# Kernel optimization log

Hardware: AMD Instinct MI355X
Metric: run time of the kernel (lower is better)

The kernel has to match this reference:

```python
import jax, jax.numpy as jnp
import numpy as np

B, H, W, C = 8, 28, 28, 1024
NH = 16
HD = C // NH
HID = 4 * C
BC = C // 2
SCALE = HD ** -0.5
EPS_LN = 1e-5   # nn.LayerNorm default
EPS_CLN = 1e-6  # detectron2 LayerNorm default


def layer_norm(x, w, b, eps=EPS_LN):
    m = jnp.mean(x, -1, keepdims=True)
    v = jnp.mean((x - m) ** 2, -1, keepdims=True)
    return (x - m) * jax.lax.rsqrt(v + eps) * w + b


def conv2d(x, w, padding):
    return jax.lax.conv_general_dilated(x, w, (1, 1), padding,
                                        dimension_numbers=("NHWC", "HWIO", "NHWC"))


def rel_table(rel_pos, size):
    # q_size == k_size, so relative index is simply (i - j) + (size - 1)
    idx = jnp.arange(size)[:, None] - jnp.arange(size)[None, :] + (size - 1)
    return rel_pos[idx]  # (size, size, HD)


def setup_inputs() -> dict:
    key = jax.random.key(0)
    ks = jax.random.split(key, 12)
    rn = lambda k, shape, s=0.02: jax.random.normal(k, shape, jnp.float32) * s
    return {
        "x": jax.random.normal(ks[0], (B, H, W, C), jnp.float32),
        "ln1_w": jnp.ones((C,), jnp.float32), "ln1_b": jnp.zeros((C,), jnp.float32),
        "qkv_w": rn(ks[1], (C, 3 * C)), "qkv_b": jnp.zeros((3 * C,), jnp.float32),
        "proj_w": rn(ks[2], (C, C)), "proj_b": jnp.zeros((C,), jnp.float32),
        "rel_pos_h": rn(ks[3], (2 * H - 1, HD)),
        "rel_pos_w": rn(ks[4], (2 * W - 1, HD)),
        "ln2_w": jnp.ones((C,), jnp.float32), "ln2_b": jnp.zeros((C,), jnp.float32),
        "mlp_w1": rn(ks[5], (C, HID)), "mlp_b1": jnp.zeros((HID,), jnp.float32),
        "mlp_w2": rn(ks[6], (HID, C)), "mlp_b2": jnp.zeros((C,), jnp.float32),
        "conv1_w": rn(ks[7], (1, 1, C, BC)),
        "cln1_w": jnp.ones((BC,), jnp.float32), "cln1_b": jnp.zeros((BC,), jnp.float32),
        "conv2_w": rn(ks[8], (3, 3, BC, BC)),
        "cln2_w": jnp.ones((BC,), jnp.float32), "cln2_b": jnp.zeros((BC,), jnp.float32),
        "conv3_w": rn(ks[9], (1, 1, BC, C)),
        "cln3_w": jnp.ones((C,), jnp.float32), "cln3_b": jnp.zeros((C,), jnp.float32),
    }


def _attention(h, qkv_w, qkv_b, proj_w, proj_b, rel_pos_h, rel_pos_w):
    # h: (B, N, C) with N = H*W
    Bq, N, _ = h.shape
    qkv = (h @ qkv_w + qkv_b).reshape(Bq, N, 3, NH, HD)
    q, k, v = jnp.moveaxis(qkv, 2, 0)          # each (B, N, NH, HD)
    q = jnp.swapaxes(q, 1, 2)                  # (B, NH, N, HD)
    k = jnp.swapaxes(k, 1, 2)
    v = jnp.swapaxes(v, 1, 2)
    attn = jnp.einsum("bhqd,bhkd->bhqk", q * SCALE, k)  # (B, NH, N, N)
    # decomposed relative position bias (uses UNscaled q, as in torch source)
    Rh = rel_table(rel_pos_h, H)               # (H, H, HD)
    Rw = rel_table(rel_pos_w, W)               # (W, W, HD)
    rq = q.reshape(Bq, NH, H, W, HD)
    rel_h = jnp.einsum("bnhwd,hkd->bnhwk", rq, Rh)  # (B, NH, H, W, H)
    rel_w = jnp.einsum("bnhwd,wkd->bnhwk", rq, Rw)  # (B, NH, H, W, W)
    attn = (attn.reshape(Bq, NH, H, W, H, W)
            + rel_h[..., :, None] + rel_w[..., None, :]).reshape(Bq, NH, N, N)
    attn = jax.nn.softmax(attn, axis=-1)
    out = jnp.einsum("bhqk,bhkd->bhqd", attn, v)     # (B, NH, N, HD)
    out = jnp.swapaxes(out, 1, 2).reshape(Bq, N, C)
    return out @ proj_w + proj_b


def reference(x, ln1_w, ln1_b, qkv_w, qkv_b, proj_w, proj_b, rel_pos_h, rel_pos_w,
              ln2_w, ln2_b, mlp_w1, mlp_b1, mlp_w2, mlp_b2,
              conv1_w, cln1_w, cln1_b, conv2_w, cln2_w, cln2_b,
              conv3_w, cln3_w, cln3_b):
    Bq = x.shape[0]
    N = H * W
    xt = x.reshape(Bq, N, C)
    shortcut = xt
    h = layer_norm(xt, ln1_w, ln1_b)
    a = _attention(h, qkv_w, qkv_b, proj_w, proj_b, rel_pos_h, rel_pos_w)
    xt = shortcut + a
    h2 = layer_norm(xt, ln2_w, ln2_b)
    mlp = jax.nn.gelu(h2 @ mlp_w1 + mlp_b1, approximate=False) @ mlp_w2 + mlp_b2
    xt = xt + mlp
    y = xt.reshape(Bq, H, W, C)
    # residual bottleneck conv block (NHWC; detectron2 LN == per-pixel channel LN)
    o = conv2d(y, conv1_w, "VALID")
    o = jax.nn.gelu(layer_norm(o, cln1_w, cln1_b, EPS_CLN), approximate=False)
    o = conv2d(o, conv2_w, "SAME")
    o = jax.nn.gelu(layer_norm(o, cln2_w, cln2_b, EPS_CLN), approximate=False)
    o = conv2d(o, conv3_w, "VALID")
    o = layer_norm(o, cln3_w, cln3_b, EPS_CLN)
    return y + o
```

## Files before the change

kernel.cpp:

```cpp
#include <hip/hip_runtime.h>
#include <hip/hip_bf16.h>

#define DI __device__ __forceinline__

typedef short bf16x8 __attribute__((ext_vector_type(8)));
typedef float f32x4 __attribute__((ext_vector_type(4)));

constexpr int BB = 8, CC = 1024, NHEAD = 16, HD = 64, HIDC = 4096, BCC = 512;
constexpr int NT = 784;
constexpr int MROWS = BB * NT;
constexpr float ATT_SCALE = 0.125f;

DI short f2bf(float f) {
    unsigned u = __builtin_bit_cast(unsigned, f);
    u = u + 0x7FFFu + ((u >> 16) & 1u);
    return (short)(u >> 16);
}
DI float bf2f(short h) {
    unsigned u = ((unsigned)(unsigned short)h) << 16;
    return __builtin_bit_cast(float, u);
}
DI float gelu_f(float x) { return 0.5f * x * (1.0f + erff(x * 0.70710678118654752f)); }

DI void gload16(const void* g, void* l) {
    __builtin_amdgcn_global_load_lds(
        (const __attribute__((address_space(1))) void*)g,
        (__attribute__((address_space(3))) void*)l, 16, 0, 0);
}

__global__ __launch_bounds__(256)
void cvt_t_kernel(const float* __restrict__ in, short* __restrict__ out, int K, int N) {
    __shared__ short t[64][68];
    const int k0 = blockIdx.y * 64, n0 = blockIdx.x * 64;
    const int tid = threadIdx.x;
    const int r = tid >> 4, c4 = (tid & 15) << 2;
    #pragma unroll
    for (int rr = 0; rr < 64; rr += 16) {
        float4 v = *(const float4*)(in + (size_t)(k0 + r + rr) * N + n0 + c4);
        t[r + rr][c4 + 0] = f2bf(v.x); t[r + rr][c4 + 1] = f2bf(v.y);
        t[r + rr][c4 + 2] = f2bf(v.z); t[r + rr][c4 + 3] = f2bf(v.w);
    }
    __syncthreads();
    #pragma unroll
    for (int rr = 0; rr < 64; rr += 16) {
        int nrow = r + rr;
        short4 o;
        o.x = t[c4 + 0][nrow]; o.y = t[c4 + 1][nrow];
        o.z = t[c4 + 2][nrow]; o.w = t[c4 + 3][nrow];
        *(short4*)(out + (size_t)(n0 + nrow) * K + k0 + c4) = o;
    }
}

__global__ void cvt_tables_kernel(const float* __restrict__ rph, const float* __restrict__ rpw,
                                  short* __restrict__ rhb, short* __restrict__ rwb) {
    int i = blockIdx.x * 256 + threadIdx.x;
    if (i < 3520) rhb[i] = f2bf(rph[i]);
    else if (i < 7040) rwb[i - 3520] = f2bf(rpw[i - 3520]);
}

template<bool GELU_, bool RESID, bool OUTBF>
__global__ void ln_kernel(const float* __restrict__ in, const float* __restrict__ gw,
                          const float* __restrict__ gb, const float* __restrict__ resid,
                          void* __restrict__ outv, int C, float eps) {
    const int row = blockIdx.x;
    const int tid = threadIdx.x;
    const float* x = in + (size_t)row * C;
    const int c4 = C >> 2;
    float s = 0.f, s2 = 0.f;
    for (int i = tid; i < c4; i += 256) {
        float4 v = ((const float4*)x)[i];
        s += v.x + v.y + v.z + v.w;
        s2 += v.x * v.x + v.y * v.y + v.z * v.z + v.w * v.w;
    }
    for (int off = 32; off; off >>= 1) { s += __shfl_xor(s, off); s2 += __shfl_xor(s2, off); }
    __shared__ float sa[4], sb[4], stats[2];
    int wid = tid >> 6;
    if ((tid & 63) == 0) { sa[wid] = s; sb[wid] = s2; }
    __syncthreads();
    if (tid == 0) {
        float S = sa[0] + sa[1] + sa[2] + sa[3];
        float S2 = sb[0] + sb[1] + sb[2] + sb[3];
        float mean = S / C;
        float var = S2 / C - mean * mean;
        stats[0] = mean; stats[1] = rsqrtf(var + eps);
    }
    __syncthreads();
    const float mean = stats[0], rstd = stats[1];
    for (int i = tid; i < c4; i += 256) {
        float4 v = ((const float4*)x)[i];
        float4 w4 = ((const float4*)gw)[i];
        float4 b4 = ((const float4*)gb)[i];
        float o[4] = { (v.x - mean) * rstd * w4.x + b4.x,
                       (v.y - mean) * rstd * w4.y + b4.y,
                       (v.z - mean) * rstd * w4.z + b4.z,
                       (v.w - mean) * rstd * w4.w + b4.w };
        if (GELU_) {
            #pragma unroll
            for (int j = 0; j < 4; j++) o[j] = gelu_f(o[j]);
        }
        if (RESID) {
            float4 r4 = ((const float4*)(resid + (size_t)row * C))[i];
            o[0] += r4.x; o[1] += r4.y; o[2] += r4.z; o[3] += r4.w;
        }
        if (OUTBF) {
            short4 ov; ov.x = f2bf(o[0]); ov.y = f2bf(o[1]); ov.z = f2bf(o[2]); ov.w = f2bf(o[3]);
            ((short4*)((short*)outv + (size_t)row * C))[i] = ov;
        } else {
            float4 ov; ov.x = o[0]; ov.y = o[1]; ov.z = o[2]; ov.w = o[3];
            ((float4*)((float*)outv + (size_t)row * C))[i] = ov;
        }
    }
}

template<bool OUTBF, bool HASB, bool ACTG, bool HASR, bool IMC, bool DUAL>
__global__ __launch_bounds__(256)
void gemm_kernel(const short* __restrict__ A, const short* __restrict__ Bt,
                 const float* __restrict__ bias, const float* __restrict__ resid,
                 void* __restrict__ outv, short* __restrict__ out2,
                 int M, int N, int K, const short* __restrict__ zg) {
    __shared__ __align__(16) short As[128 * 32];
    __shared__ __align__(16) short Bs[128 * 32];
    const int tid = threadIdx.x;
    const int nwg = gridDim.x * gridDim.y;
    const int orig = blockIdx.y * gridDim.x + blockIdx.x;
    const int qq = nwg >> 3, rr8 = nwg & 7;
    const int xcd = orig & 7, loc = orig >> 3;
    const int wg = (xcd < rr8 ? xcd * (qq + 1) : rr8 * (qq + 1) + (xcd - rr8) * qq) + loc;
    const int m0 = (wg / gridDim.x) * 128, n0 = (wg % gridDim.x) * 128;
    const int lane = tid & 63, wid = tid >> 6;
    const int wr = (wid >> 1) * 64, wc = (wid & 1) * 64;
    const int lr = lane & 15, lkb = lane >> 4;

    const int srow = lane >> 2;
    const int schunk = lane & 3;

    const short* aptr[2];
    const short* bptr[2];
    short* adst[2]; short* bdst[2];
    int ihh[2], iww[2], ioff[2];
    const short* ibase[2];

    #pragma unroll
    for (int i = 0; i < 2; i++) {
        int seg = wid * 2 + i;
        int row = seg * 16 + srow;
        int c = schunk ^ (row & 3);
        adst[i] = As + seg * 512;
        bdst[i] = Bs + seg * 512;
        bptr[i] = Bt + (size_t)(n0 + row) * K + c * 8;
        if (!IMC) {
            aptr[i] = A + (size_t)(m0 + row) * K + c * 8;
        } else {
            int m = m0 + row;
            int bimg = m / 784, rem = m - bimg * 784;
            ihh[i] = rem / 28; iww[i] = rem - (rem / 28) * 28;
            ibase[i] = A + (size_t)bimg * 784 * 512;
            ioff[i] = c * 8;
        }
    }

    f32x4 acc[4][4];
    #pragma unroll
    for (int i = 0; i < 4; i++)
        #pragma unroll
        for (int j = 0; j < 4; j++) acc[i][j] = f32x4{0.f, 0.f, 0.f, 0.f};

    const int pc = (lkb ^ (lr & 3)) << 3;
    const int nkt = K >> 5;
    for (int kt = 0; kt < nkt; ++kt) {
        if (!IMC) {
            #pragma unroll
            for (int i = 0; i < 2; i++) {
                gload16(aptr[i] + kt * 32, adst[i]);
                gload16(bptr[i] + kt * 32, bdst[i]);
            }
        } else {
            int segk = kt >> 4;
            int ky = segk / 3, kx = segk - ky * 3;
            int ccb = (kt & 15) << 5;
            #pragma unroll
            for (int i = 0; i < 2; i++) {
                int ih = ihh[i] + ky - 1, iw = iww[i] + kx - 1;
                bool ok = (ih >= 0) & (ih < 28) & (iw >= 0) & (iw < 28);
                const short* s = ok ? ibase[i] + ((size_t)(ih * 28 + iw) * 512 + ccb + ioff[i]) : zg;
                gload16(s, adst[i]);
                gload16(bptr[i] + kt * 32, bdst[i]);
            }
        }
        __syncthreads();
        bf16x8 af[4], bfv[4];
        #pragma unroll
        for (int mt = 0; mt < 4; mt++) af[mt] = *(const bf16x8*)&As[(wr + mt * 16 + lr) * 32 + pc];
        #pragma unroll
        for (int nt = 0; nt < 4; nt++) bfv[nt] = *(const bf16x8*)&Bs[(wc + nt * 16 + lr) * 32 + pc];
        #pragma unroll
        for (int mt = 0; mt < 4; mt++)
            #pragma unroll
            for (int nt = 0; nt < 4; nt++)
                acc[mt][nt] = __builtin_amdgcn_mfma_f32_16x16x32_bf16(af[mt], bfv[nt], acc[mt][nt], 0, 0, 0);
        __syncthreads();
    }
    const int ro = (lane >> 4) << 2;
    #pragma unroll
    for (int mt = 0; mt < 4; mt++) {
        #pragma unroll
        for (int nt = 0; nt < 4; nt++) {
            int col = n0 + wc + nt * 16 + lr;
            float bv = HASB ? bias[col] : 0.0f;
            #pragma unroll
            for (int j = 0; j < 4; j++) {
                int row = m0 + wr + mt * 16 + ro + j;
                float v = acc[mt][nt][j] + bv;
                if (ACTG) v = gelu_f(v);
                size_t oi = (size_t)row * N + col;
                if (HASR) v += resid[oi];
                if (OUTBF) ((short*)outv)[oi] = f2bf(v);
                else       ((float*)outv)[oi] = v;
                if (DUAL)  out2[oi] = f2bf(v);
            }
        }
    }
}

__global__ __launch_bounds__(64)
void relpos_mfma_kernel(const short* __restrict__ qkv, const short* __restrict__ rhb,
                        const short* __restrict__ rwb, float* __restrict__ relh,
                        float* __restrict__ relw) {
    const int p = blockIdx.x;
    const int bh = blockIdx.y;
    const int mode = blockIdx.z;
    const int bimg = bh >> 4, nh = bh & 15;
    const int lane = threadIdx.x;
    const int lr = lane & 15, lkb = lane >> 4;
    const short* rb = mode ? rwb : rhb;
    float* outp = mode ? relw : relh;

    bf16x8 afr[2][2];
    #pragma unroll
    for (int mt = 0; mt < 2; mt++) {
        int kh = mt * 16 + lr;
        int sr = p - kh + 27;
        sr = sr < 0 ? 0 : (sr > 54 ? 54 : sr);
        #pragma unroll
        for (int ks = 0; ks < 2; ks++)
            afr[mt][ks] = *(const bf16x8*)(rb + sr * 64 + ks * 32 + lkb * 8);
    }
    bf16x8 bfq[2][2];
    #pragma unroll
    for (int nt = 0; nt < 2; nt++) {
        int cc = nt * 16 + lr;
        int nlin = mode ? (cc * 28 + p) : (p * 28 + cc);
        if (nlin > 783) nlin = 783;
        const short* qp = qkv + (size_t)(bimg * 784 + nlin) * 3072 + nh * 64;
        #pragma unroll
        for (int ks = 0; ks < 2; ks++)
            bfq[nt][ks] = *(const bf16x8*)(qp + ks * 32 + lkb * 8);
    }
    f32x4 acc[2][2];
    #pragma unroll
    for (int i = 0; i < 2; i++)
        #pragma unroll
        for (int j = 0; j < 2; j++) acc[i][j] = f32x4{0.f, 0.f, 0.f, 0.f};
    #pragma unroll
    for (int ks = 0; ks < 2; ks++)
        #pragma unroll
        for (int mt = 0; mt < 2; mt++)
            #pragma unroll
            for (int nt = 0; nt < 2; nt++)
                acc[mt][nt] = __builtin_amdgcn_mfma_f32_16x16x32_bf16(afr[mt][ks], bfq[nt][ks], acc[mt][nt], 0, 0, 0);
    const int ro = lkb << 2;
    #pragma unroll
    for (int nt = 0; nt < 2; nt++) {
        int cc = nt * 16 + lr;
        if (cc < 28) {
            int nlin = mode ? (cc * 28 + p) : (p * 28 + cc);
            float* o = outp + ((size_t)bh * 784 + nlin) * 28;
            *(f32x4*)(o + ro) = acc[0][nt];
            if (ro < 12) *(f32x4*)(o + 16 + ro) = acc[1][nt];
        }
    }
}

__global__ __launch_bounds__(256)
void attn_kernel(const short* __restrict__ qkv, const float* __restrict__ relh,
                 const float* __restrict__ relw, short* __restrict__ outp) {
    constexpr int VSTR = 34;
    __shared__ __align__(16) short Ks[32 * 64];
    __shared__ __align__(16) short Vt[64 * VSTR];
    __shared__ __align__(16) short Pl[4][16 * 40];
    __shared__ float relS[4][16 * 57];
    const int qb = blockIdx.x;
    const int bh = blockIdx.y;
    const int bimg = bh >> 4, nh = bh & 15;
    const int tid = threadIdx.x;
    const int lane = tid & 63, wid = tid >> 6;
    const int lr = lane & 15, lkb = lane >> 4;
    const int lk = lkb * 8;
    const int qw0 = qb * 64 + wid * 16;

    for (int idx = lane; idx < 16 * 56; idx += 64) {
        int qq = idx / 56, j = idx - qq * 56;
        int n = qw0 + qq; if (n > 783) n = 783;
        relS[wid][qq * 57 + j] = (j < 28) ? relh[((size_t)bh * 784 + n) * 28 + j]
                                          : relw[((size_t)bh * 784 + n) * 28 + (j - 28)];
    }
    bf16x8 bq0, bq1;
    {
        int tok = qw0 + lr; if (tok > 783) tok = 783;
        const short* qp = qkv + (size_t)(bimg * 784 + tok) * 3072 + nh * 64;
        bq0 = *(const bf16x8*)(qp + lk);
        bq1 = *(const bf16x8*)(qp + 32 + lk);
    }
    f32x4 oacc[4];
    #pragma unroll
    for (int i = 0; i < 4; i++) oacc[i] = f32x4{0.f, 0.f, 0.f, 0.f};
    float m_run = -1e30f, l_run = 0.0f;

    const int krow = tid >> 3, kcp = tid & 7;
    const int kclog = kcp ^ (krow & 7);
    short* kdst = Ks + wid * 512;
    const int vkey = tid & 31, vdb = tid >> 5;
    const int kq4 = lkb << 2;

    for (int kt = 0; kt < 25; ++kt) {
        const int k0 = kt * 32;
        {
            int key = k0 + krow; if (key > 783) key = 783;
            gload16(qkv + (size_t)(bimg * 784 + key) * 3072 + 1024 + nh * 64 + kclog * 8, kdst);
        }
        {
            int key = k0 + vkey; if (key > 783) key = 783;
            bf16x8 vv = *(const bf16x8*)(qkv + (size_t)(bimg * 784 + key) * 3072 + 2048 + nh * 64 + vdb * 8);
            #pragma unroll
            for (int j = 0; j < 8; j++) Vt[(vdb * 8 + j) * VSTR + vkey] = vv[j];
        }
        __syncthreads();
        f32x4 sacc[2];
        sacc[0] = f32x4{0.f, 0.f, 0.f, 0.f}; sacc[1] = f32x4{0.f, 0.f, 0.f, 0.f};
        #pragma unroll
        for (int mb = 0; mb < 2; mb++) {
            int row = mb * 16 + lr;
            bf16x8 ak0 = *(const bf16x8*)&Ks[row * 64 + ((lkb ^ (row & 7)) << 3)];
            bf16x8 ak1 = *(const bf16x8*)&Ks[row * 64 + (((4 + lkb) ^ (row & 7)) << 3)];
            sacc[mb] = __builtin_amdgcn_mfma_f32_16x16x32_bf16(ak0, bq0, sacc[mb], 0, 0, 0);
            sacc[mb] = __builtin_amdgcn_mfma_f32_16x16x32_bf16(ak1, bq1, sacc[mb], 0, 0, 0);
        }
        float sv[8];
        #pragma unroll
        for (int mb = 0; mb < 2; mb++)
            #pragma unroll
            for (int j = 0; j < 4; j++) {
                int key = k0 + mb * 16 + kq4 + j;
                float v;
                if (key < 784) {
                    int h2 = key / 28, w2 = key - (key / 28) * 28;
                    v = sacc[mb][j] * ATT_SCALE + relS[wid][lr * 57 + h2] + relS[wid][lr * 57 + 28 + w2];
                } else v = -1e30f;
                sv[mb * 4 + j] = v;
            }
        float mt_ = sv[0];
        #pragma unroll
        for (int i = 1; i < 8; i++) mt_ = fmaxf(mt_, sv[i]);
        mt_ = fmaxf(mt_, __shfl_xor(mt_, 16));
        mt_ = fmaxf(mt_, __shfl_xor(mt_, 32));
        if (__all(mt_ - m_run <= 8.0f)) {
            float psum = 0.f;
            #pragma unroll
            for (int i = 0; i < 8; i++) {
                float pz = __expf(sv[i] - m_run);
                psum += pz;
                Pl[wid][lr * 40 + ((i >> 2) * 16 + kq4 + (i & 3))] = f2bf(pz);
            }
            psum += __shfl_xor(psum, 16);
            psum += __shfl_xor(psum, 32);
            l_run += psum;
        } else {
            float mnew = fmaxf(m_run, mt_);
            float corr = __expf(m_run - mnew);
            float psum = 0.f;
            #pragma unroll
            for (int i = 0; i < 8; i++) {
                float pz = __expf(sv[i] - mnew);
                psum += pz;
                Pl[wid][lr * 40 + ((i >> 2) * 16 + kq4 + (i & 3))] = f2bf(pz);
            }
            psum += __shfl_xor(psum, 16);
            psum += __shfl_xor(psum, 32);
            l_run = l_run * corr + psum;
            m_run = mnew;
            #pragma unroll
            for (int db = 0; db < 4; db++) {
                f32x4 t = oacc[db];
                t[0] *= corr; t[1] *= corr; t[2] *= corr; t[3] *= corr;
                oacc[db] = t;
            }
        }
        bf16x8 pb = *(const bf16x8*)&Pl[wid][lr * 40 + lk];
        #pragma unroll
        for (int db = 0; db < 4; db++) {
            bf16x8 av = *(const bf16x8*)&Vt[(db * 16 + lr) * VSTR + lk];
            oacc[db] = __builtin_amdgcn_mfma_f32_16x16x32_bf16(av, pb, oacc[db], 0, 0, 0);
        }
        __syncthreads();
    }
    const float inv = 1.0f / l_run;
    const int tok = qw0 + lr;
    if (tok < 784) {
        short* op = outp + (size_t)(bimg * 784 + tok) * 1024 + nh * 64;
        #pragma unroll
        for (int db = 0; db < 4; db++)
            #pragma unroll
            for (int j = 0; j < 4; j++) {
                int d = db * 16 + kq4 + j;
                op[d] = f2bf(oacc[db][j] * inv);
            }
    }
}

extern "C" void kernel_launch(void* const* d_in, const int* in_sizes, int n_in,
                              void* d_out, int out_size, void* d_ws, size_t ws_size,
                              hipStream_t stream) {
    const float* x      = (const float*)d_in[0];
    const float* ln1w   = (const float*)d_in[1];
    const float* ln1b   = (const float*)d_in[2];
    const float* qkvw   = (const float*)d_in[3];
    const float* qkvbia = (const float*)d_in[4];
    const float* projw  = (const float*)d_in[5];
    const float* projb  = (const float*)d_in[6];
    const float* rph    = (const float*)d_in[7];
    const float* rpw    = (const float*)d_in[8];
    const float* ln2w   = (const float*)d_in[9];
    const float* ln2b   = (const float*)d_in[10];
    const float* m1w    = (const float*)d_in[11];
    const float* m1b    = (const float*)d_in[12];
    const float* m2w    = (const float*)d_in[13];
    const float* m2b    = (const float*)d_in[14];
    const float* c1w    = (const float*)d_in[15];
    const float* cl1w   = (const float*)d_in[16];
    const float* cl1b   = (const float*)d_in[17];
    const float* c2w    = (const float*)d_in[18];
    const float* cl2w   = (const float*)d_in[19];
    const float* cl2b   = (const float*)d_in[20];
    const float* c3w    = (const float*)d_in[21];
    const float* cl3w   = (const float*)d_in[22];
    const float* cl3b   = (const float*)d_in[23];
    float* out = (float*)d_out;

    char* base = (char*)d_ws;
    size_t off = 0;
    auto alloc = [&](size_t bytes) -> char* {
        char* p = base + off;
        off = (off + bytes + 255) & ~(size_t)255;
        return p;
    };
    short* wq  = (short*)alloc((size_t)3072 * 1024 * 2);
    short* wp  = (short*)alloc((size_t)1024 * 1024 * 2);
    short* w1  = (short*)alloc((size_t)4096 * 1024 * 2);
    short* w2  = (short*)alloc((size_t)1024 * 4096 * 2);
    short* wc1 = (short*)alloc((size_t)512 * 1024 * 2);
    short* wc2 = (short*)alloc((size_t)512 * 4608 * 2);
    short* wc3 = (short*)alloc((size_t)1024 * 512 * 2);
    short* hbuf = (short*)alloc((size_t)MROWS * 1024 * 2);
    short* qkvb = (short*)alloc((size_t)MROWS * 3072 * 2);
    float* relh = (float*)alloc((size_t)128 * 784 * 28 * 4);
    float* relw = (float*)alloc((size_t)128 * 784 * 28 * 4);
    float* xt   = (float*)alloc((size_t)MROWS * 1024 * 4);
    short* hid  = (short*)alloc((size_t)MROWS * 4096 * 2);
    float* yf   = (float*)alloc((size_t)MROWS * 1024 * 4);
    short* zg   = (short*)alloc(256);
    short* rhb  = (short*)alloc(3520 * 2);
    short* rwb  = (short*)alloc(3520 * 2);
    (void)relw; (void)ws_size; (void)in_sizes; (void)n_in; (void)out_size;

    float* o1f  = (float*)hid;
    short* o1g  = (short*)((char*)hid + (size_t)MROWS * 512 * 4);
    float* o2f  = (float*)((char*)o1g + (size_t)MROWS * 512 * 2);
    short* o2g  = (short*)((char*)o2f + (size_t)MROWS * 512 * 4);
    float* o3f  = (float*)qkvb;
    short* ybf  = (short*)relh;

    hipMemsetAsync(zg, 0, 256, stream);

    auto cvtT = [&](const float* src, short* dst, int K, int N) {
        cvt_t_kernel<<<dim3(N / 64, K / 64), 256, 0, stream>>>(src, dst, K, N);
    };
    cvtT(qkvw, wq, 1024, 3072);
    cvtT(projw, wp, 1024, 1024);
    cvtT(m1w, w1, 1024, 4096);
    cvtT(m2w, w2, 4096, 1024);
    cvtT(c1w, wc1, 1024, 512);
    cvtT(c2w, wc2, 4608, 512);
    cvtT(c3w, wc3, 512, 1024);
    cvt_tables_kernel<<<28, 256, 0, stream>>>(rph, rpw, rhb, rwb);

    ln_kernel<false, false, true><<<MROWS, 256, 0, stream>>>(x, ln1w, ln1b, nullptr, hbuf, 1024, 1e-5f);
    gemm_kernel<true, true, false, false, false, false><<<dim3(24, 49), 256, 0, stream>>>(
        hbuf, wq, qkvbia, nullptr, qkvb, nullptr, MROWS, 3072, 1024, zg);
    relpos_mfma_kernel<<<dim3(28, 128, 2), 64, 0, stream>>>(qkvb, rhb, rwb, relh, relw);
    attn_kernel<<<dim3(13, 128), 256, 0, stream>>>(qkvb, relh, relw, hbuf);
    gemm_kernel<false, true, false, true, false, false><<<dim3(8, 49), 256, 0, stream>>>(
        hbuf, wp, projb, x, xt, nullptr, MROWS, 1024, 1024, zg);
    ln_kernel<false, false, true><<<MROWS, 256, 0, stream>>>(xt, ln2w, ln2b, nullptr, hbuf, 1024, 1e-5f);
    gemm_kernel<true, true, true, false, false, false><<<dim3(32, 49), 256, 0, stream>>>(
        hbuf, w1, m1b, nullptr, hid, nullptr, MROWS, 4096, 1024, zg);
    gemm_kernel<false, true, false, true, false, true><<<dim3(8, 49), 256, 0, stream>>>(
        hid, w2, m2b, xt, yf, ybf, MROWS, 1024, 4096, zg);
    gemm_kernel<false, false, false, false, false, false><<<dim3(4, 49), 256, 0, stream>>>(
        ybf, wc1, nullptr, nullptr, o1f, nullptr, MROWS, 512, 1024, zg);
    ln_kernel<true, false, true><<<MROWS, 256, 0, stream>>>(o1f, cl1w, cl1b, nullptr, o1g, 512, 1e-6f);
    gemm_kernel<false, false, false, false, true, false><<<dim3(4, 49), 256, 0, stream>>>(
        o1g, wc2, nullptr, nullptr, o2f, nullptr, MROWS, 512, 4608, zg);
    ln_kernel<true, false, true><<<MROWS, 256, 0, stream>>>(o2f, cl2w, cl2b, nullptr, o2g, 512, 1e-6f);
    gemm_kernel<false, false, false, false, false, false><<<dim3(8, 49), 256, 0, stream>>>(
        o2g, wc3, nullptr, nullptr, o3f, nullptr, MROWS, 1024, 512, zg);
    ln_kernel<false, true, false><<<MROWS, 256, 0, stream>>>(o3f, cl3w, cl3b, yf, out, 1024, 1e-6f);
}
```

Before: 773.7 us.

## Double-buffer GEMM LDS tiles to overlap global loads with MFMA

Doubles the shared-memory A/B tiles and restructures the GEMM main loop so the next K-slice is issued via direct-to-LDS loads before computing on the current buffer. A partial vmcnt wait replaces the full sync, letting one tile's loads stay in flight during MFMA work. This aims to hide global memory latency in every GEMM (linear layers and implicit conv), at the cost of twice the LDS per block, which may lower occupancy. It also relies on hand-placed waitcnt and barrier ordering being correct.

```diff
diff --git a/kernel.cpp b/kernel.cpp
--- a/kernel.cpp
+++ b/kernel.cpp
@@ -118,8 +118,8 @@
                  const float* __restrict__ bias, const float* __restrict__ resid,
                  void* __restrict__ outv, short* __restrict__ out2,
                  int M, int N, int K, const short* __restrict__ zg) {
-    __shared__ __align__(16) short As[128 * 32];
-    __shared__ __align__(16) short Bs[128 * 32];
+    __shared__ __align__(16) short As[2 * 128 * 32];
+    __shared__ __align__(16) short Bs[2 * 128 * 32];
     const int tid = threadIdx.x;
     const int nwg = gridDim.x * gridDim.y;
     const int orig = blockIdx.y * gridDim.x + blockIdx.x;
@@ -136,7 +136,7 @@
 
     const short* aptr[2];
     const short* bptr[2];
-    short* adst[2]; short* bdst[2];
+    int sdst[2];
     int ihh[2], iww[2], ioff[2];
     const short* ibase[2];
 
@@ -145,8 +145,7 @@
         int seg = wid * 2 + i;
         int row = seg * 16 + srow;
         int c = schunk ^ (row & 3);
-        adst[i] = As + seg * 512;
-        bdst[i] = Bs + seg * 512;
+        sdst[i] = seg * 512;
         bptr[i] = Bt + (size_t)(n0 + row) * K + c * 8;
         if (!IMC) {
             aptr[i] = A + (size_t)(m0 + row) * K + c * 8;
@@ -159,20 +158,14 @@
         }
     }
 
-    f32x4 acc[4][4];
-    #pragma unroll
-    for (int i = 0; i < 4; i++)
-        #pragma unroll
-        for (int j = 0; j < 4; j++) acc[i][j] = f32x4{0.f, 0.f, 0.f, 0.f};
-
-    const int pc = (lkb ^ (lr & 3)) << 3;
-    const int nkt = K >> 5;
-    for (int kt = 0; kt < nkt; ++kt) {
+    auto stage = [&](int kt, int buf) {
+        short* ab = As + buf * 4096;
+        short* bb = Bs + buf * 4096;
         if (!IMC) {
             #pragma unroll
             for (int i = 0; i < 2; i++) {
-                gload16(aptr[i] + kt * 32, adst[i]);
-                gload16(bptr[i] + kt * 32, bdst[i]);
+                gload16(aptr[i] + kt * 32, ab + sdst[i]);
+                gload16(bptr[i] + kt * 32, bb + sdst[i]);
             }
         } else {
             int segk = kt >> 4;
@@ -183,22 +176,47 @@
                 int ih = ihh[i] + ky - 1, iw = iww[i] + kx - 1;
                 bool ok = (ih >= 0) & (ih < 28) & (iw >= 0) & (iw < 28);
                 const short* s = ok ? ibase[i] + ((size_t)(ih * 28 + iw) * 512 + ccb + ioff[i]) : zg;
-                gload16(s, adst[i]);
-                gload16(bptr[i] + kt * 32, bdst[i]);
-            }
-        }
-        __syncthreads();
+                gload16(s, ab + sdst[i]);
+                gload16(bptr[i] + kt * 32, bb + sdst[i]);
+            }
+        }
+    };
+
+    f32x4 acc[4][4];
+    #pragma unroll
+    for (int i = 0; i < 4; i++)
+        #pragma unroll
+        for (int j = 0; j < 4; j++) acc[i][j] = f32x4{0.f, 0.f, 0.f, 0.f};
+
+    const int pc = (lkb ^ (lr & 3)) << 3;
+    const int nkt = K >> 5;
+    int cur = 0;
+    stage(0, 0);
+    for (int kt = 0; kt < nkt; ++kt) {
+        if (kt + 1 < nkt) {
+            stage(kt + 1, cur ^ 1);
+            asm volatile("s_waitcnt vmcnt(4)" ::: "memory");
+        } else {
+            asm volatile("s_waitcnt vmcnt(0)" ::: "memory");
+        }
+        __builtin_amdgcn_sched_barrier(0);
+        __builtin_amdgcn_s_barrier();
+        __builtin_amdgcn_sched_barrier(0);
+        const short* ab = As + cur * 4096;
+        const short* bb = Bs + cur * 4096;
         bf16x8 af[4], bfv[4];
         #pragma unroll
-        for (int mt = 0; mt < 4; mt++) af[mt] = *(const bf16x8*)&As[(wr + mt * 16 + lr) * 32 + pc];
-        #pragma unroll
-        for (int nt = 0; nt < 4; nt++) bfv[nt] = *(const bf16x8*)&Bs[(wc + nt * 16 + lr) * 32 + pc];
+        for (int mt = 0; mt < 4; mt++) af[mt] = *(const bf16x8*)&ab[(wr + mt * 16 + lr) * 32 + pc];
+        #pragma unroll
+        for (int nt = 0; nt < 4; nt++) bfv[nt] = *(const bf16x8*)&bb[(wc + nt * 16 + lr) * 32 + pc];
         #pragma unroll
         for (int mt = 0; mt < 4; mt++)
             #pragma unroll
             for (int nt = 0; nt < 4; nt++)
                 acc[mt][nt] = __builtin_amdgcn_mfma_f32_16x16x32_bf16(af[mt], bfv[nt], acc[mt][nt], 0, 0, 0);
-        __syncthreads();
+        __builtin_amdgcn_s_barrier();
+        __builtin_amdgcn_sched_barrier(0);
+        cur ^= 1;
     }
     const int ro = (lane >> 4) << 2;
     #pragma unroll
```

Result: faster. 731.9 us (-5.4%).
